# Kernel optimization log

Measured on AMD Instinct MI355X. Metric: run time of the kernel, lower is better.

Reference implementation:

```python
import jax, jax.numpy as jnp
import numpy as np

E, K = 8, 2            # num_experts, top_k
D, H = 1024, 4096      # d_model, expert_hidden_dim
B, S = 4, 2048         # batch, seq
AUX_W = 0.01


def setup_inputs() -> dict:
    key = jax.random.key(0)
    k0, k1, k2, k3 = jax.random.split(key, 4)
    return {
        "x": jax.random.normal(k0, (B, S, D), jnp.float32),
        "router_w": jax.random.normal(k1, (D, E), jnp.float32) * 0.02,  # normal(0.02) init per MoERouter
        "router_b": jnp.zeros((E,), jnp.float32),
        "w_up": jax.random.normal(k2, (E, D, H), jnp.float32) * (1.0 / np.sqrt(D)),
        "b_up": jnp.zeros((E, H), jnp.float32),
        "w_down": jax.random.normal(k3, (E, H, D), jnp.float32) * (1.0 / np.sqrt(H)),
        "b_down": jnp.zeros((E, D), jnp.float32),
    }


def reference(x, router_w, router_b, w_up, b_up, w_down, b_down):
    # Router
    logits = x @ router_w + router_b                       # (B,S,E)
    router_probs = jax.nn.softmax(logits, axis=-1)         # (B,S,E)
    topk_logits, topk_idx = jax.lax.top_k(logits, K)       # (B,S,K)
    topk_p = jax.nn.softmax(topk_logits, axis=-1)          # (B,S,K)

    # Dense all-expert MLP (matches original: every expert computed on every token)
    h = jax.nn.gelu(jnp.einsum('bsd,edh->bseh', x, w_up) + b_up)   # (B,S,E,H)
    all_out = jnp.einsum('bseh,ehd->bsed', h, w_down) + b_down     # (B,S,E,D)

    # Top-k gather + weighted combine
    sel = jnp.take_along_axis(all_out, topk_idx[..., None], axis=2)  # (B,S,K,D)
    output = jnp.sum(topk_p[..., None] * sel, axis=2)                # (B,S,D)

    # Load-balancing aux loss (Switch/Mixtral formulation)
    counts = jnp.zeros((E,), jnp.float32).at[topk_idx.reshape(-1)].add(1.0)
    fraction = counts / (B * S * K)
    prob_mean = router_probs.mean(axis=(0, 1))
    aux_loss = E * jnp.sum(fraction * prob_mean) * AUX_W
    return output, aux_loss, router_probs
```

## Files before the change

kernel.cpp:

```cpp
#include <hip/hip_runtime.h>
#include <hip/hip_bf16.h>
#include <stdint.h>

constexpr int NT = 8192;
constexpr int NE = 8;
constexpr int ND = 1024;
constexpr int NH = 4096;

typedef __attribute__((ext_vector_type(8))) short short8;
typedef __attribute__((ext_vector_type(4))) float f32x4;

constexpr size_t O_XBF  = 0;
constexpr size_t O_WUPT = O_XBF  + (size_t)NT * ND * 2;
constexpr size_t O_WDNT = O_WUPT + (size_t)NE * NH * ND * 2;
constexpr size_t O_HBUF = O_WDNT + (size_t)NE * ND * NH * 2;
constexpr size_t O_STOK = O_HBUF + (size_t)NT * 2 * NH * 2;
constexpr size_t O_SP   = O_STOK + (size_t)NT * 2 * 4;
constexpr size_t O_TKE  = O_SP   + (size_t)NT * 2 * 4;
constexpr size_t O_TKP  = O_TKE  + (size_t)NT * 2 * 4;
constexpr size_t O_CTRL = O_TKP  + (size_t)NT * 2 * 4;
constexpr size_t O_TLUP = O_CTRL + 272;
constexpr size_t O_TLDN = O_TLUP + 144 * 4;

__device__ __forceinline__ void gl_lds16(const void* g, void* l) {
  using GP = char __attribute__((address_space(1))) *;
  using LP = char __attribute__((address_space(3))) *;
  __builtin_amdgcn_global_load_lds((GP)(uintptr_t)g, (LP)(uint32_t)(uintptr_t)l, 16, 0, 0);
}

__device__ __forceinline__ float fast_gelu(float x) {
  float u  = 0.7978845608028654f * (x + 0.044715f * x * x * x);
  float ex = __expf(2.0f * u);
  float th = 1.0f - 2.0f / (ex + 1.0f);
  return 0.5f * x * (1.0f + th);
}

__global__ __launch_bounds__(256) void moe_router(
    const float* __restrict__ x, const float* __restrict__ rw, const float* __restrict__ rb,
    __hip_bfloat16* __restrict__ xbf,
    float* __restrict__ probs_out, int* __restrict__ topk_e, float* __restrict__ topk_p,
    int* __restrict__ cnt_ek, float* __restrict__ probsum)
{
  __shared__ float ps[NE];
  __shared__ int cs[16];
  const int tid = threadIdx.x;
  if (tid < NE) ps[tid] = 0.f;
  if (tid < 16) cs[tid] = 0;
  __syncthreads();
  const int lane = tid & 63, wv = tid >> 6;
  for (int it = 0; it < 8; ++it) {
    const int t = blockIdx.x * 4 + wv + it * 1024;
    const float* xr = x + (size_t)t * ND;
    float acc[NE] = {};
#pragma unroll 4
    for (int j = 0; j < 16; ++j) {
      const int d = j * 64 + lane;
      const float xv = xr[d];
      xbf[(size_t)t * ND + d] = __float2bfloat16(xv);
      const float* w = rw + (size_t)d * NE;
#pragma unroll
      for (int ee = 0; ee < NE; ++ee) acc[ee] += xv * w[ee];
    }
#pragma unroll
    for (int ee = 0; ee < NE; ++ee)
#pragma unroll
      for (int off = 32; off >= 1; off >>= 1)
        acc[ee] += __shfl_down(acc[ee], off, 64);
    if (lane == 0) {
      float lg[NE];
#pragma unroll
      for (int ee = 0; ee < NE; ++ee) lg[ee] = acc[ee] + rb[ee];
      float mx = lg[0];
#pragma unroll
      for (int ee = 1; ee < NE; ++ee) mx = fmaxf(mx, lg[ee]);
      float s = 0.f, pe[NE];
#pragma unroll
      for (int ee = 0; ee < NE; ++ee) { pe[ee] = __expf(lg[ee] - mx); s += pe[ee]; }
      const float inv = 1.f / s;
#pragma unroll
      for (int ee = 0; ee < NE; ++ee) {
        const float pr = pe[ee] * inv;
        probs_out[(size_t)t * NE + ee] = pr;
        atomicAdd(&ps[ee], pr);
      }
      int i1 = 0; float l1 = lg[0];
#pragma unroll
      for (int ee = 1; ee < NE; ++ee) if (lg[ee] > l1) { l1 = lg[ee]; i1 = ee; }
      int i2 = 0; float l2 = -3.0e38f;
#pragma unroll
      for (int ee = 0; ee < NE; ++ee) if (ee != i1 && lg[ee] > l2) { l2 = lg[ee]; i2 = ee; }
      const float e2 = __expf(l2 - l1);
      const float dn = 1.f + e2;
      topk_e[t * 2]     = i1;  topk_e[t * 2 + 1] = i2;
      topk_p[t * 2]     = 1.f / dn;
      topk_p[t * 2 + 1] = e2 / dn;
      atomicAdd(&cs[i1 * 2], 1);
      atomicAdd(&cs[i2 * 2 + 1], 1);
    }
  }
  __syncthreads();
  if (tid < NE) atomicAdd(&probsum[tid], ps[tid]);
  if (tid < 16) atomicAdd(&cnt_ek[tid], cs[tid]);
}

__global__ void moe_finalize(const int* __restrict__ cnt_ek, int* __restrict__ off_ek,
                             const float* __restrict__ probsum, float* __restrict__ aux_out,
                             int* __restrict__ ntiles, int* __restrict__ tl_up,
                             int* __restrict__ tl_dn)
{
  if (threadIdx.x == 0 && blockIdx.x == 0) {
    int run = 0;
    for (int i = 0; i < 16; ++i) { off_ek[i] = run; run += cnt_ek[i]; }
    float aux = 0.f;
    for (int ee = 0; ee < NE; ++ee) {
      float frac = (float)(cnt_ek[2 * ee] + cnt_ek[2 * ee + 1]) / (float)(NT * 2);
      aux += frac * (probsum[ee] / (float)NT);
    }
    aux_out[0] = (float)NE * aux * 0.01f;
    int ntu = 0;
    for (int e = 0; e < NE; ++e) {
      const int c = cnt_ek[2 * e] + cnt_ek[2 * e + 1];
      for (int mb = 0; mb < (c + 127) / 128; ++mb) tl_up[ntu++] = (e << 16) | mb;
    }
    ntiles[0] = ntu;
    for (int kp = 0; kp < 2; ++kp) {
      int nt = 0;
      for (int e = 0; e < NE; ++e) {
        const int c = cnt_ek[2 * e + kp];
        for (int mb = 0; mb < (c + 127) / 128; ++mb) tl_dn[kp * 80 + nt++] = (e << 16) | mb;
      }
      ntiles[1 + kp] = nt;
    }
  }
}

__global__ __launch_bounds__(256) void moe_scatter(
    const int* __restrict__ topk_e, const float* __restrict__ topk_p,
    const int* __restrict__ off_ek, int* __restrict__ fill_ek,
    int* __restrict__ slot_token, float* __restrict__ slot_p)
{
  const int t = blockIdx.x * 256 + threadIdx.x;
  if (t >= NT) return;
#pragma unroll
  for (int k = 0; k < 2; ++k) {
    const int ee = topk_e[t * 2 + k];
    const int id = ee * 2 + k;
    const int r = atomicAdd(&fill_ek[id], 1);
    const int slot = off_ek[id] + r;
    slot_token[slot] = t;
    slot_p[slot] = topk_p[t * 2 + k];
  }
}

__global__ __launch_bounds__(256) void moe_transpose_cast(
    const float* __restrict__ in, __hip_bfloat16* __restrict__ outp, int Adim, int Bdim)
{
  __shared__ unsigned short tile[64 * 66];
  const int e = blockIdx.z;
  const int b0 = blockIdx.x * 64, a0 = blockIdx.y * 64;
  const float* ip = in + (size_t)e * Adim * Bdim + (size_t)a0 * Bdim + b0;
  const int c4 = (threadIdx.x & 15) * 4;
  const int r0 = threadIdx.x >> 4;
#pragma unroll
  for (int i = 0; i < 4; ++i) {
    const int r = r0 + i * 16;
    const float4 v = *(const float4*)(ip + (size_t)r * Bdim + c4);
    ushort4 u;
    u.x = __hip_bfloat16_raw(__float2bfloat16(v.x)).x;
    u.y = __hip_bfloat16_raw(__float2bfloat16(v.y)).x;
    u.z = __hip_bfloat16_raw(__float2bfloat16(v.z)).x;
    u.w = __hip_bfloat16_raw(__float2bfloat16(v.w)).x;
    *(ushort4*)&tile[r * 66 + c4] = u;
  }
  __syncthreads();
  unsigned short* op = (unsigned short*)outp + (size_t)e * Bdim * Adim + (size_t)b0 * Adim + a0;
  const int cc  = threadIdx.x >> 2;
  const int rr0 = (threadIdx.x & 3) * 16;
  unsigned short u[16];
#pragma unroll
  for (int i = 0; i < 16; ++i) u[i] = tile[(rr0 + i) * 66 + cc];
  *(short8*)(op + (size_t)cc * Adim + rr0)     = *(short8*)&u[0];
  *(short8*)(op + (size_t)cc * Adim + rr0 + 8) = *(short8*)&u[8];
}

__global__ __launch_bounds__(512, 5) void moe_gemm_up(
    const __hip_bfloat16* __restrict__ xbf,
    const __hip_bfloat16* __restrict__ wupT,
    const float* __restrict__ b_up,
    const int* __restrict__ slot_token,
    const int* __restrict__ cnt_ek, const int* __restrict__ off_ek,
    const int* __restrict__ ntiles, const int* __restrict__ tl_up,
    __hip_bfloat16* __restrict__ hbuf)
{
  if ((int)blockIdx.y >= ntiles[0]) return;
  const int tl = tl_up[blockIdx.y];
  const int e = tl >> 16, mb = tl & 0xffff;
  const int cnt = cnt_ek[2 * e] + cnt_ek[2 * e + 1];
  const int base = off_ek[2 * e];
  const int m0 = mb * 128;
  const int n0 = blockIdx.x * 128;
  const int valid = (cnt - m0 < 128) ? (cnt - m0) : 128;

  __shared__ __align__(16) __hip_bfloat16 As[128 * 32];
  __shared__ __align__(16) __hip_bfloat16 Bs[128 * 32];

  const int tid = threadIdx.x;
  const int lane = tid & 63, wv = tid >> 6;

  const int ra = tid >> 2;
  const int kc = ((tid & 3) ^ ((ra >> 1) & 3)) * 8;
  const int sa = base + ((m0 + ra < cnt) ? (m0 + ra) : (cnt - 1));
  const __hip_bfloat16* ga = xbf + (size_t)slot_token[sa] * ND + kc;
  const __hip_bfloat16* gb = wupT + ((size_t)e * NH + n0 + ra) * ND + kc;
  char* lA = (char*)As + tid * 16;
  char* lB = (char*)Bs + tid * 16;

  const int wm = (wv >> 2) * 64, wn = (wv & 3) * 32;
  const int l15 = lane & 15, q = lane >> 4;
  const int ssw = (q ^ ((l15 >> 1) & 3)) * 16;
  const char* rA = (const char*)As + (wm + l15) * 64 + ssw;
  const char* rB = (const char*)Bs + (wn + l15) * 64 + ssw;

  f32x4 acc[4][2] = {};

  for (int kk = 0; kk < ND; kk += 32) {
    __syncthreads();
    gl_lds16(ga + kk, lA);
    gl_lds16(gb + kk, lB);
    __syncthreads();
    short8 af[4], bfr[2];
#pragma unroll
    for (int i = 0; i < 4; ++i) af[i]  = *(const short8*)(rA + i * 1024);
#pragma unroll
    for (int i = 0; i < 2; ++i) bfr[i] = *(const short8*)(rB + i * 1024);
#pragma unroll
    for (int mt = 0; mt < 4; ++mt)
#pragma unroll
      for (int nt = 0; nt < 2; ++nt)
        acc[mt][nt] = __builtin_amdgcn_mfma_f32_16x16x32_bf16(af[mt], bfr[nt], acc[mt][nt], 0, 0, 0);
  }

#pragma unroll
  for (int mt = 0; mt < 4; ++mt) {
#pragma unroll
    for (int rr = 0; rr < 4; ++rr) {
      const int row = wm + mt * 16 + q * 4 + rr;
      if (row < valid) {
        const size_t rbase = (size_t)(base + m0 + row) * NH;
#pragma unroll
        for (int nt = 0; nt < 2; ++nt) {
          const int col = n0 + wn + nt * 16 + l15;
          const float v = acc[mt][nt][rr] + b_up[e * NH + col];
          hbuf[rbase + col] = __float2bfloat16(fast_gelu(v));
        }
      }
    }
  }
}

__global__ __launch_bounds__(512, 5) void moe_gemm_down(
    const __hip_bfloat16* __restrict__ hbuf,
    const __hip_bfloat16* __restrict__ wdnT,
    const float* __restrict__ b_down,
    const int* __restrict__ slot_token, const float* __restrict__ slot_p,
    const int* __restrict__ cnt_ek, const int* __restrict__ off_ek,
    const int* __restrict__ ntiles, const int* __restrict__ tl_dn,
    float* __restrict__ out, int kpos)
{
  if ((int)blockIdx.y >= ntiles[1 + kpos]) return;
  const int tl = tl_dn[kpos * 80 + blockIdx.y];
  const int e = tl >> 16, mb = tl & 0xffff;
  const int id = 2 * e + kpos;
  const int cnt = cnt_ek[id];
  const int base = off_ek[id];
  const int m0 = mb * 128;
  const int n0 = blockIdx.x * 128;
  const int valid = (cnt - m0 < 128) ? (cnt - m0) : 128;

  __shared__ __align__(16) __hip_bfloat16 As[128 * 32];
  __shared__ __align__(16) __hip_bfloat16 Bs[128 * 32];

  const int tid = threadIdx.x;
  const int lane = tid & 63, wv = tid >> 6;

  const int ra = tid >> 2;
  const int kc = ((tid & 3) ^ ((ra >> 1) & 3)) * 8;
  const int sa = base + ((m0 + ra < cnt) ? (m0 + ra) : (cnt - 1));
  const __hip_bfloat16* ga = hbuf + (size_t)sa * NH + kc;
  const __hip_bfloat16* gb = wdnT + ((size_t)e * ND + n0 + ra) * NH + kc;
  char* lA = (char*)As + tid * 16;
  char* lB = (char*)Bs + tid * 16;

  const int wm = (wv >> 2) * 64, wn = (wv & 3) * 32;
  const int l15 = lane & 15, q = lane >> 4;
  const int ssw = (q ^ ((l15 >> 1) & 3)) * 16;
  const char* rA = (const char*)As + (wm + l15) * 64 + ssw;
  const char* rB = (const char*)Bs + (wn + l15) * 64 + ssw;

  f32x4 acc[4][2] = {};

  for (int kk = 0; kk < NH; kk += 32) {
    __syncthreads();
    gl_lds16(ga + kk, lA);
    gl_lds16(gb + kk, lB);
    __syncthreads();
    short8 af[4], bfr[2];
#pragma unroll
    for (int i = 0; i < 4; ++i) af[i]  = *(const short8*)(rA + i * 1024);
#pragma unroll
    for (int i = 0; i < 2; ++i) bfr[i] = *(const short8*)(rB + i * 1024);
#pragma unroll
    for (int mt = 0; mt < 4; ++mt)
#pragma unroll
      for (int nt = 0; nt < 2; ++nt)
        acc[mt][nt] = __builtin_amdgcn_mfma_f32_16x16x32_bf16(af[mt], bfr[nt], acc[mt][nt], 0, 0, 0);
  }

#pragma unroll
  for (int mt = 0; mt < 4; ++mt) {
#pragma unroll
    for (int rr = 0; rr < 4; ++rr) {
      const int row = wm + mt * 16 + q * 4 + rr;
      if (row < valid) {
        const int slot = base + m0 + row;
        const int tok = slot_token[slot];
        const float p = slot_p[slot];
        const size_t obase = (size_t)tok * ND;
#pragma unroll
        for (int nt = 0; nt < 2; ++nt) {
          const int col = n0 + wn + nt * 16 + l15;
          const float v = (acc[mt][nt][rr] + b_down[e * ND + col]) * p;
          if (kpos == 0) out[obase + col] = v;
          else           out[obase + col] += v;
        }
      }
    }
  }
}

extern "C" void kernel_launch(void* const* d_in, const int* in_sizes, int n_in,
                              void* d_out, int out_size, void* d_ws, size_t ws_size,
                              hipStream_t stream) {
  (void)in_sizes; (void)n_in; (void)out_size; (void)ws_size;
  const float* x   = (const float*)d_in[0];
  const float* rw  = (const float*)d_in[1];
  const float* rb  = (const float*)d_in[2];
  const float* wup = (const float*)d_in[3];
  const float* bup = (const float*)d_in[4];
  const float* wdn = (const float*)d_in[5];
  const float* bdn = (const float*)d_in[6];
  float* out = (float*)d_out;

  char* ws = (char*)d_ws;
  __hip_bfloat16* xbf  = (__hip_bfloat16*)(ws + O_XBF);
  __hip_bfloat16* wupT = (__hip_bfloat16*)(ws + O_WUPT);
  __hip_bfloat16* wdnT = (__hip_bfloat16*)(ws + O_WDNT);
  __hip_bfloat16* hbuf = (__hip_bfloat16*)(ws + O_HBUF);
  int*   slot_token = (int*)(ws + O_STOK);
  float* slot_p     = (float*)(ws + O_SP);
  int*   topk_e     = (int*)(ws + O_TKE);
  float* topk_p     = (float*)(ws + O_TKP);
  int*   cnt_ek  = (int*)(ws + O_CTRL);
  int*   fill_ek = (int*)(ws + O_CTRL + 64);
  float* probsum = (float*)(ws + O_CTRL + 128);
  int*   off_ek  = (int*)(ws + O_CTRL + 192);
  int*   ntiles  = (int*)(ws + O_CTRL + 256);
  int*   tl_up   = (int*)(ws + O_TLUP);
  int*   tl_dn   = (int*)(ws + O_TLDN);

  hipMemsetAsync(ws + O_CTRL, 0, 272, stream);

  moe_transpose_cast<<<dim3(NH / 64, ND / 64, NE), 256, 0, stream>>>(wup, wupT, ND, NH);
  moe_transpose_cast<<<dim3(ND / 64, NH / 64, NE), 256, 0, stream>>>(wdn, wdnT, NH, ND);

  moe_router<<<256, 256, 0, stream>>>(x, rw, rb, xbf, out + (size_t)NT * ND + 1,
                                      topk_e, topk_p, cnt_ek, probsum);
  moe_finalize<<<1, 64, 0, stream>>>(cnt_ek, off_ek, probsum, out + (size_t)NT * ND,
                                     ntiles, tl_up, tl_dn);
  moe_scatter<<<NT / 256, 256, 0, stream>>>(topk_e, topk_p, off_ek, fill_ek, slot_token, slot_p);

  moe_gemm_up<<<dim3(NH / 128, 144, 1), 512, 0, stream>>>(xbf, wupT, bup, slot_token,
                                                          cnt_ek, off_ek, ntiles, tl_up, hbuf);
  moe_gemm_down<<<dim3(ND / 128, 80, 1), 512, 0, stream>>>(hbuf, wdnT, bdn, slot_token, slot_p,
                                                           cnt_ek, off_ek, ntiles, tl_dn, out, 0);
  moe_gemm_down<<<dim3(ND / 128, 80, 1), 512, 0, stream>>>(hbuf, wdnT, bdn, slot_token, slot_p,
                                                           cnt_ek, off_ek, ntiles, tl_dn, out, 1);
}
```

Before: 933.2 us.

## Widen GEMM N-tile to 256, merge down-proj launches with atomics, parallelize scatter/finalize

Both expert GEMMs move from 128x128 to 128x256 tiles, with each wave computing a 64x64 sub-tile (4x4 MFMA accumulators), to raise operand reuse per LDS load. The two per-k down-projection launches become one launch that accumulates into a zeroed output with float atomicAdd. The scatter kernel aggregates counts per block in shared memory before touching the global counters, and the finalize kernel writes its tile lists in parallel. The wider tiles cut the number of blocks and increase register pressure; the float atomics make the sum order nondeterministic and require an extra memset of the output.

```diff
diff --git a/kernel.cpp b/kernel.cpp
--- a/kernel.cpp
+++ b/kernel.cpp
@@ -6,6 +6,10 @@
 constexpr int NE = 8;
 constexpr int ND = 1024;
 constexpr int NH = 4096;
+
+constexpr int TM = 128;
+constexpr int TN = 256;
+constexpr int BK = 32;
 
 typedef __attribute__((ext_vector_type(8))) short short8;
 typedef __attribute__((ext_vector_type(4))) float f32x4;
@@ -20,7 +24,7 @@
 constexpr size_t O_TKP  = O_TKE  + (size_t)NT * 2 * 4;
 constexpr size_t O_CTRL = O_TKP  + (size_t)NT * 2 * 4;
 constexpr size_t O_TLUP = O_CTRL + 272;
-constexpr size_t O_TLDN = O_TLUP + 144 * 4;
+constexpr size_t O_TLDN = O_TLUP + 160 * 4;
 
 __device__ __forceinline__ void gl_lds16(const void* g, void* l) {
   using GP = char __attribute__((address_space(1))) *;
@@ -108,29 +112,39 @@
                              int* __restrict__ ntiles, int* __restrict__ tl_up,
                              int* __restrict__ tl_dn)
 {
-  if (threadIdx.x == 0 && blockIdx.x == 0) {
+  __shared__ int c[16], off[16], uoff[8], ucnt[8], doff[16], dcnt[16];
+  const int tid = threadIdx.x;
+  if (tid < 16) c[tid] = cnt_ek[tid];
+  __syncthreads();
+  if (tid == 0) {
     int run = 0;
-    for (int i = 0; i < 16; ++i) { off_ek[i] = run; run += cnt_ek[i]; }
+    for (int i = 0; i < 16; ++i) { off[i] = run; run += c[i]; }
+    int ur = 0;
+    for (int e = 0; e < NE; ++e) {
+      ucnt[e] = (c[2 * e] + c[2 * e + 1] + TM - 1) / TM;
+      uoff[e] = ur; ur += ucnt[e];
+    }
+    ntiles[0] = ur;
+    int dr = 0;
+    for (int i = 0; i < 16; ++i) {
+      dcnt[i] = (c[i] + TM - 1) / TM;
+      doff[i] = dr; dr += dcnt[i];
+    }
+    ntiles[1] = dr;
     float aux = 0.f;
-    for (int ee = 0; ee < NE; ++ee) {
-      float frac = (float)(cnt_ek[2 * ee] + cnt_ek[2 * ee + 1]) / (float)(NT * 2);
-      aux += frac * (probsum[ee] / (float)NT);
+    for (int e = 0; e < NE; ++e) {
+      float frac = (float)(c[2 * e] + c[2 * e + 1]) / (float)(NT * 2);
+      aux += frac * (probsum[e] / (float)NT);
     }
     aux_out[0] = (float)NE * aux * 0.01f;
-    int ntu = 0;
-    for (int e = 0; e < NE; ++e) {
-      const int c = cnt_ek[2 * e] + cnt_ek[2 * e + 1];
-      for (int mb = 0; mb < (c + 127) / 128; ++mb) tl_up[ntu++] = (e << 16) | mb;
-    }
-    ntiles[0] = ntu;
-    for (int kp = 0; kp < 2; ++kp) {
-      int nt = 0;
-      for (int e = 0; e < NE; ++e) {
-        const int c = cnt_ek[2 * e + kp];
-        for (int mb = 0; mb < (c + 127) / 128; ++mb) tl_dn[kp * 80 + nt++] = (e << 16) | mb;
-      }
-      ntiles[1 + kp] = nt;
-    }
+  }
+  __syncthreads();
+  if (tid < 16) off_ek[tid] = off[tid];
+  if (tid < 8)
+    for (int mb = 0; mb < ucnt[tid]; ++mb) tl_up[uoff[tid] + mb] = (tid << 16) | mb;
+  if (tid >= 32 && tid < 48) {
+    const int i = tid - 32;
+    for (int mb = 0; mb < dcnt[i]; ++mb) tl_dn[doff[i] + mb] = (i << 16) | mb;
   }
 }
 
@@ -139,16 +153,33 @@
     const int* __restrict__ off_ek, int* __restrict__ fill_ek,
     int* __restrict__ slot_token, float* __restrict__ slot_p)
 {
-  const int t = blockIdx.x * 256 + threadIdx.x;
-  if (t >= NT) return;
-#pragma unroll
-  for (int k = 0; k < 2; ++k) {
-    const int ee = topk_e[t * 2 + k];
-    const int id = ee * 2 + k;
-    const int r = atomicAdd(&fill_ek[id], 1);
-    const int slot = off_ek[id] + r;
+  __shared__ int lc[16], gb[16], offs[16];
+  const int tid = threadIdx.x;
+  if (tid < 16) lc[tid] = 0;
+  __syncthreads();
+  const int t = blockIdx.x * 256 + tid;
+  const int id0 = topk_e[t * 2] * 2;
+  const int id1 = topk_e[t * 2 + 1] * 2 + 1;
+  atomicAdd(&lc[id0], 1);
+  atomicAdd(&lc[id1], 1);
+  __syncthreads();
+  if (tid < 16) {
+    gb[tid] = atomicAdd(&fill_ek[tid], lc[tid]);
+    offs[tid] = off_ek[tid];
+    lc[tid] = 0;
+  }
+  __syncthreads();
+  {
+    const int r = atomicAdd(&lc[id0], 1);
+    const int slot = offs[id0] + gb[id0] + r;
     slot_token[slot] = t;
-    slot_p[slot] = topk_p[t * 2 + k];
+    slot_p[slot] = topk_p[t * 2];
+  }
+  {
+    const int r = atomicAdd(&lc[id1], 1);
+    const int slot = offs[id1] + gb[id1] + r;
+    slot_token[slot] = t;
+    slot_p[slot] = topk_p[t * 2 + 1];
   }
 }
 
@@ -183,7 +214,7 @@
   *(short8*)(op + (size_t)cc * Adim + rr0 + 8) = *(short8*)&u[8];
 }
 
-__global__ __launch_bounds__(512, 5) void moe_gemm_up(
+__global__ __launch_bounds__(512, 4) void moe_gemm_up(
     const __hip_bfloat16* __restrict__ xbf,
     const __hip_bfloat16* __restrict__ wupT,
     const float* __restrict__ b_up,
@@ -197,49 +228,60 @@
   const int e = tl >> 16, mb = tl & 0xffff;
   const int cnt = cnt_ek[2 * e] + cnt_ek[2 * e + 1];
   const int base = off_ek[2 * e];
-  const int m0 = mb * 128;
-  const int n0 = blockIdx.x * 128;
-  const int valid = (cnt - m0 < 128) ? (cnt - m0) : 128;
-
-  __shared__ __align__(16) __hip_bfloat16 As[128 * 32];
-  __shared__ __align__(16) __hip_bfloat16 Bs[128 * 32];
+  const int m0 = mb * TM;
+  const int n0 = blockIdx.x * TN;
+  const int valid = (cnt - m0 < TM) ? (cnt - m0) : TM;
+
+  __shared__ __align__(16) __hip_bfloat16 As[TM * BK];
+  __shared__ __align__(16) __hip_bfloat16 Bs[TN * BK];
 
   const int tid = threadIdx.x;
   const int lane = tid & 63, wv = tid >> 6;
 
-  const int ra = tid >> 2;
-  const int kc = ((tid & 3) ^ ((ra >> 1) & 3)) * 8;
-  const int sa = base + ((m0 + ra < cnt) ? (m0 + ra) : (cnt - 1));
-  const __hip_bfloat16* ga = xbf + (size_t)slot_token[sa] * ND + kc;
-  const __hip_bfloat16* gb = wupT + ((size_t)e * NH + n0 + ra) * ND + kc;
+  const int raA = tid >> 2;
+  const int kcA = ((tid & 3) ^ ((raA >> 1) & 3)) * 8;
+  int srA = m0 + raA; if (srA >= cnt) srA = cnt - 1;
+  const __hip_bfloat16* ga = xbf + (size_t)slot_token[base + srA] * ND + kcA;
+  const __hip_bfloat16* gb[2];
+#pragma unroll
+  for (int j = 0; j < 2; ++j) {
+    const int ci = tid + 512 * j;
+    const int row = ci >> 2;
+    const int kc = ((ci & 3) ^ ((row >> 1) & 3)) * 8;
+    gb[j] = wupT + ((size_t)e * NH + n0 + row) * ND + kc;
+  }
   char* lA = (char*)As + tid * 16;
   char* lB = (char*)Bs + tid * 16;
 
-  const int wm = (wv >> 2) * 64, wn = (wv & 3) * 32;
+  const int wm = (wv >> 2) * 64, wn = (wv & 3) * 64;
   const int l15 = lane & 15, q = lane >> 4;
   const int ssw = (q ^ ((l15 >> 1) & 3)) * 16;
   const char* rA = (const char*)As + (wm + l15) * 64 + ssw;
   const char* rB = (const char*)Bs + (wn + l15) * 64 + ssw;
 
-  f32x4 acc[4][2] = {};
-
-  for (int kk = 0; kk < ND; kk += 32) {
+  f32x4 acc[4][4] = {};
+
+  for (int kk = 0; kk < ND; kk += BK) {
     __syncthreads();
     gl_lds16(ga + kk, lA);
-    gl_lds16(gb + kk, lB);
+    gl_lds16(gb[0] + kk, lB);
+    gl_lds16(gb[1] + kk, lB + 8192);
     __syncthreads();
-    short8 af[4], bfr[2];
+    short8 af[4], bfr[4];
 #pragma unroll
     for (int i = 0; i < 4; ++i) af[i]  = *(const short8*)(rA + i * 1024);
 #pragma unroll
-    for (int i = 0; i < 2; ++i) bfr[i] = *(const short8*)(rB + i * 1024);
+    for (int i = 0; i < 4; ++i) bfr[i] = *(const short8*)(rB + i * 1024);
 #pragma unroll
     for (int mt = 0; mt < 4; ++mt)
 #pragma unroll
-      for (int nt = 0; nt < 2; ++nt)
+      for (int nt = 0; nt < 4; ++nt)
         acc[mt][nt] = __builtin_amdgcn_mfma_f32_16x16x32_bf16(af[mt], bfr[nt], acc[mt][nt], 0, 0, 0);
   }
 
+  float bias[4];
+#pragma unroll
+  for (int nt = 0; nt < 4; ++nt) bias[nt] = b_up[e * NH + n0 + wn + nt * 16 + l15];
 #pragma unroll
   for (int mt = 0; mt < 4; ++mt) {
 #pragma unroll
@@ -248,74 +290,84 @@
       if (row < valid) {
         const size_t rbase = (size_t)(base + m0 + row) * NH;
 #pragma unroll
-        for (int nt = 0; nt < 2; ++nt) {
+        for (int nt = 0; nt < 4; ++nt) {
           const int col = n0 + wn + nt * 16 + l15;
-          const float v = acc[mt][nt][rr] + b_up[e * NH + col];
-          hbuf[rbase + col] = __float2bfloat16(fast_gelu(v));
+          hbuf[rbase + col] = __float2bfloat16(fast_gelu(acc[mt][nt][rr] + bias[nt]));
         }
       }
     }
   }
 }
 
-__global__ __launch_bounds__(512, 5) void moe_gemm_down(
+__global__ __launch_bounds__(512, 4) void moe_gemm_down(
     const __hip_bfloat16* __restrict__ hbuf,
     const __hip_bfloat16* __restrict__ wdnT,
     const float* __restrict__ b_down,
     const int* __restrict__ slot_token, const float* __restrict__ slot_p,
     const int* __restrict__ cnt_ek, const int* __restrict__ off_ek,
     const int* __restrict__ ntiles, const int* __restrict__ tl_dn,
-    float* __restrict__ out, int kpos)
-{
-  if ((int)blockIdx.y >= ntiles[1 + kpos]) return;
-  const int tl = tl_dn[kpos * 80 + blockIdx.y];
-  const int e = tl >> 16, mb = tl & 0xffff;
-  const int id = 2 * e + kpos;
+    float* __restrict__ out)
+{
+  if ((int)blockIdx.y >= ntiles[1]) return;
+  const int tl = tl_dn[blockIdx.y];
+  const int id = tl >> 16, mb = tl & 0xffff;
+  const int e = id >> 1;
   const int cnt = cnt_ek[id];
   const int base = off_ek[id];
-  const int m0 = mb * 128;
-  const int n0 = blockIdx.x * 128;
-  const int valid = (cnt - m0 < 128) ? (cnt - m0) : 128;
-
-  __shared__ __align__(16) __hip_bfloat16 As[128 * 32];
-  __shared__ __align__(16) __hip_bfloat16 Bs[128 * 32];
+  const int m0 = mb * TM;
+  const int n0 = blockIdx.x * TN;
+  const int valid = (cnt - m0 < TM) ? (cnt - m0) : TM;
+
+  __shared__ __align__(16) __hip_bfloat16 As[TM * BK];
+  __shared__ __align__(16) __hip_bfloat16 Bs[TN * BK];
 
   const int tid = threadIdx.x;
   const int lane = tid & 63, wv = tid >> 6;
 
-  const int ra = tid >> 2;
-  const int kc = ((tid & 3) ^ ((ra >> 1) & 3)) * 8;
-  const int sa = base + ((m0 + ra < cnt) ? (m0 + ra) : (cnt - 1));
-  const __hip_bfloat16* ga = hbuf + (size_t)sa * NH + kc;
-  const __hip_bfloat16* gb = wdnT + ((size_t)e * ND + n0 + ra) * NH + kc;
+  const int raA = tid >> 2;
+  const int kcA = ((tid & 3) ^ ((raA >> 1) & 3)) * 8;
+  int srA = m0 + raA; if (srA >= cnt) srA = cnt - 1;
+  const __hip_bfloat16* ga = hbuf + (size_t)(base + srA) * NH + kcA;
+  const __hip_bfloat16* gb[2];
+#pragma unroll
+  for (int j = 0; j < 2; ++j) {
+    const int ci = tid + 512 * j;
+    const int row = ci >> 2;
+    const int kc = ((ci & 3) ^ ((row >> 1) & 3)) * 8;
+    gb[j] = wdnT + ((size_t)e * ND + n0 + row) * NH + kc;
+  }
   char* lA = (char*)As + tid * 16;
   char* lB = (char*)Bs + tid * 16;
 
-  const int wm = (wv >> 2) * 64, wn = (wv & 3) * 32;
+  const int wm = (wv >> 2) * 64, wn = (wv & 3) * 64;
   const int l15 = lane & 15, q = lane >> 4;
   const int ssw = (q ^ ((l15 >> 1) & 3)) * 16;
   const char* rA = (const char*)As + (wm + l15) * 64 + ssw;
   const char* rB = (const char*)Bs + (wn + l15) * 64 + ssw;
 
-  f32x4 acc[4][2] = {};
-
-  for (int kk = 0; kk < NH; kk += 32) {
+  f32x4 acc[4][4] = {};
+
+  for (int kk = 0; kk < NH; kk += BK) {
     __syncthreads();
     gl_lds16(ga + kk, lA);
-    gl_lds16(gb + kk, lB);
+    gl_lds16(gb[0] + kk, lB);
+    gl_lds16(gb[1] + kk, lB + 8192);
     __syncthreads();
-    short8 af[4], bfr[2];
+    short8 af[4], bfr[4];
 #pragma unroll
     for (int i = 0; i < 4; ++i) af[i]  = *(const short8*)(rA + i * 1024);
 #pragma unroll
-    for (int i = 0; i < 2; ++i) bfr[i] = *(const short8*)(rB + i * 1024);
+    for (int i = 0; i < 4; ++i) bfr[i] = *(const short8*)(rB + i * 1024);
 #pragma unroll
     for (int mt = 0; mt < 4; ++mt)
 #pragma unroll
-      for (int nt = 0; nt < 2; ++nt)
+      for (int nt = 0; nt < 4; ++nt)
         acc[mt][nt] = __builtin_amdgcn_mfma_f32_16x16x32_bf16(af[mt], bfr[nt], acc[mt][nt], 0, 0, 0);
   }
 
+  float bias[4];
+#pragma unroll
+  for (int nt = 0; nt < 4; ++nt) bias[nt] = b_down[e * ND + n0 + wn + nt * 16 + l15];
 #pragma unroll
   for (int mt = 0; mt < 4; ++mt) {
 #pragma unroll
@@ -327,11 +379,9 @@
         const float p = slot_p[slot];
         const size_t obase = (size_t)tok * ND;
 #pragma unroll
-        for (int nt = 0; nt < 2; ++nt) {
+        for (int nt = 0; nt < 4; ++nt) {
           const int col = n0 + wn + nt * 16 + l15;
-          const float v = (acc[mt][nt][rr] + b_down[e * ND + col]) * p;
-          if (kpos == 0) out[obase + col] = v;
-          else           out[obase + col] += v;
+          atomicAdd(&out[obase + col], (acc[mt][nt][rr] + bias[nt]) * p);
         }
       }
     }
@@ -369,6 +419,7 @@
   int*   tl_dn   = (int*)(ws + O_TLDN);
 
   hipMemsetAsync(ws + O_CTRL, 0, 272, stream);
+  hipMemsetAsync(out, 0, (size_t)NT * ND * sizeof(float), stream);
 
   moe_transpose_cast<<<dim3(NH / 64, ND / 64, NE), 256, 0, stream>>>(wup, wupT, ND, NH);
   moe_transpose_cast<<<dim3(ND / 64, NH / 64, NE), 256, 0, stream>>>(wdn, wdnT, NH, ND);
@@ -379,10 +430,8 @@
                                      ntiles, tl_up, tl_dn);
   moe_scatter<<<NT / 256, 256, 0, stream>>>(topk_e, topk_p, off_ek, fill_ek, slot_token, slot_p);
 
-  moe_gemm_up<<<dim3(NH / 128, 144, 1), 512, 0, stream>>>(xbf, wupT, bup, slot_token,
-                                                          cnt_ek, off_ek, ntiles, tl_up, hbuf);
-  moe_gemm_down<<<dim3(ND / 128, 80, 1), 512, 0, stream>>>(hbuf, wdnT, bdn, slot_token, slot_p,
-                                                           cnt_ek, off_ek, ntiles, tl_dn, out, 0);
-  moe_gemm_down<<<dim3(ND / 128, 80, 1), 512, 0, stream>>>(hbuf, wdnT, bdn, slot_token, slot_p,
-                                                           cnt_ek, off_ek, ntiles, tl_dn, out, 1);
-}
+  moe_gemm_up<<<dim3(NH / TN, 136, 1), 512, 0, stream>>>(
+      xbf, wupT, bup, slot_token, cnt_ek, off_ek, ntiles, tl_up, hbuf);
+  moe_gemm_down<<<dim3(ND / TN, 144, 1), 512, 0, stream>>>(
+      hbuf, wdnT, bdn, slot_token, slot_p, cnt_ek, off_ek, ntiles, tl_dn, out);
+}
```

Result: faster. 913.7 us (-2.1%).
